# Optimization experiments

Measured on AMD Instinct MI355X. Metric: run time of the kernel, lower is better.

The kernel has to match this reference:

```python
import jax, jax.numpy as jnp
import numpy as np

D_IN = 4097   # 4096 obj feat + 1 depth
D_H1 = 512
D_H2 = 256
N_HEADS = 4
D_HEAD = D_H2 // N_HEADS
D_FF = 512


def setup_inputs() -> dict:
    key = jax.random.key(0)
    ks = jax.random.split(key, 20)
    B, T, N = 2, 100, 30
    s = lambda *sh: 1.0 / np.sqrt(sh[0])
    inp = {
        "object_features": jax.random.normal(ks[0], (B, T, N, 4096), jnp.float32),
        "object_depths": jax.random.uniform(ks[1], (B, T, N, 1), jnp.float32),
        # spatial encoder (2-layer fully-connected message passing)
        "W1a": jax.random.normal(ks[2], (D_IN, D_H1), jnp.float32) * s(D_IN),
        "W2a": jax.random.normal(ks[3], (D_IN, D_H1), jnp.float32) * s(D_IN),
        "b1a": jnp.zeros((D_H1,), jnp.float32),
        "W1b": jax.random.normal(ks[4], (D_H1, D_H2), jnp.float32) * s(D_H1),
        "W2b": jax.random.normal(ks[5], (D_H1, D_H2), jnp.float32) * s(D_H1),
        "b1b": jnp.zeros((D_H2,), jnp.float32),
        # temporal transformer encoder layer (post-LN)
        "Wq": jax.random.normal(ks[6], (D_H2, D_H2), jnp.float32) * s(D_H2),
        "Wk": jax.random.normal(ks[7], (D_H2, D_H2), jnp.float32) * s(D_H2),
        "Wv": jax.random.normal(ks[8], (D_H2, D_H2), jnp.float32) * s(D_H2),
        "Wo": jax.random.normal(ks[9], (D_H2, D_H2), jnp.float32) * s(D_H2),
        "ln1_g": jnp.ones((D_H2,), jnp.float32),
        "ln1_b": jnp.zeros((D_H2,), jnp.float32),
        "Wf1": jax.random.normal(ks[10], (D_H2, D_FF), jnp.float32) * s(D_H2),
        "bf1": jnp.zeros((D_FF,), jnp.float32),
        "Wf2": jax.random.normal(ks[11], (D_FF, D_H2), jnp.float32) * s(D_FF),
        "bf2": jnp.zeros((D_H2,), jnp.float32),
        "ln2_g": jnp.ones((D_H2,), jnp.float32),
        "ln2_b": jnp.zeros((D_H2,), jnp.float32),
        # classifier
        "Wc": jax.random.normal(ks[12], (D_H2, 1), jnp.float32) * s(D_H2),
        "bc": jnp.zeros((1,), jnp.float32),
    }
    return inp


def _layer_norm(x, g, b, eps=1e-5):
    mu = jnp.mean(x, axis=-1, keepdims=True)
    var = jnp.var(x, axis=-1, keepdims=True)
    return (x - mu) * jax.lax.rsqrt(var + eps) * g + b


def _forward(object_features, object_depths, W1a, W2a, b1a, W1b, W2b, b1b,
             Wq, Wk, Wv, Wo, ln1_g, ln1_b, Wf1, bf1, Wf2, bf2, ln2_g, ln2_b,
             Wc, bc):
    B, T, N, _ = object_features.shape
    x = jnp.concatenate([object_features, object_depths], axis=-1)  # (B,T,N,4097)
    # fully-connected graph (torch.combinations, both directions):
    # aggregated message for node i = mean over all j != i.
    def mp(h, Ws, Wn, b):
        neigh = (jnp.sum(h, axis=2, keepdims=True) - h) / (N - 1)
        return jax.nn.relu(h @ Ws + neigh @ Wn + b)
    h = mp(x, W1a, W2a, b1a)      # (B,T,N,512)
    h = mp(h, W1b, W2b, b1b)      # (B,T,N,256)
    g = jnp.mean(h, axis=2)       # global mean pool -> (B,T,256)
    # temporal transformer encoder (self-attention over T, post-LN)
    q = (g @ Wq).reshape(B, T, N_HEADS, D_HEAD)
    k = (g @ Wk).reshape(B, T, N_HEADS, D_HEAD)
    v = (g @ Wv).reshape(B, T, N_HEADS, D_HEAD)
    scores = jnp.einsum("bthd,bshd->bhts", q, k) / np.sqrt(D_HEAD)
    attn = jax.nn.softmax(scores, axis=-1)
    ctx = jnp.einsum("bhts,bshd->bthd", attn, v).reshape(B, T, D_H2) @ Wo
    y = _layer_norm(g + ctx, ln1_g, ln1_b)
    ff = jax.nn.relu(y @ Wf1 + bf1) @ Wf2 + bf2
    z = _layer_norm(y + ff, ln2_g, ln2_b)  # (B,T,256)
    # dropout is identity in eval mode -> probs2 == probs, uncertainty == 0
    logits = (z @ Wc + bc).squeeze(-1)     # (B,T)
    probs = jax.nn.sigmoid(logits)
    uncertainty = jnp.zeros_like(probs)
    return probs, uncertainty


def reference(object_features, object_depths, W1a, W2a, b1a, W1b, W2b, b1b,
              Wq, Wk, Wv, Wo, ln1_g, ln1_b, Wf1, bf1, Wf2, bf2, ln2_g, ln2_b,
              Wc, bc):
    return _forward(object_features, object_depths, W1a, W2a, b1a, W1b, W2b,
                    b1b, Wq, Wk, Wv, Wo, ln1_g, ln1_b, Wf1, bf1, Wf2, bf2,
                    ln2_g, ln2_b, Wc, bc)
```

## Files before the change

kernel.cpp:

```cpp
#include <hip/hip_runtime.h>
#include <hip/hip_bf16.h>
#include <stdint.h>

typedef unsigned short u16;
typedef __attribute__((ext_vector_type(8))) short short8;
typedef __attribute__((ext_vector_type(4))) float floatx4;

#define BT 200
#define NOBJ 30
#define KP2 4224
#define DIN 4097
#define DH1 512
#define DH2 256
#define DFF 512
#define MPAD 6016
#define CHZ 176
#define NBIGW (132*16)
#define NSMALL 512
#define NCONV (BT*12)
#define NZERO 128

__device__ __forceinline__ u16 f2bf(float f) {
    union { float f; uint32_t u; } c; c.f = f;
    uint32_t u = c.u;
    u += 0x7FFF + ((u >> 16) & 1);
    return (u16)(u >> 16);
}

__device__ __forceinline__ void load16_lds(const u16* g, u16* l) {
    __builtin_amdgcn_global_load_lds(
        (const __attribute__((address_space(1))) void*)g,
        (__attribute__((address_space(3))) void*)l, 16, 0, 0);
}

__device__ __forceinline__ size_t tile_off(int ytile, int row, int c8) {
    int z = c8 / CHZ, rem = c8 - z * CHZ;
    int i = rem >> 3, kw = rem & 7;
    int ks = kw ^ (row & 7);
    return ((((size_t)(ytile * 3 + z) * 22 + i) * 128 + row) * 64) + ks * 8;
}

__global__ void prep_all(const float* __restrict__ W1a, const float* __restrict__ W2a,
                         const float* __restrict__ W1b, const float* __restrict__ W2b,
                         const float* __restrict__ feat, const float* __restrict__ depth,
                         u16* __restrict__ Wc1T, u16* __restrict__ W2aTs,
                         u16* __restrict__ Wc2T, u16* __restrict__ W2bTs,
                         u16* __restrict__ XbT, u16* __restrict__ SbT,
                         float* __restrict__ zeroBase, size_t zeroQuads) {
    __shared__ float t1[32][33];
    __shared__ float t2[32][33];
    int bid = blockIdx.x, tid = threadIdx.x;
    if (bid < NBIGW) {
        int kb = (bid % 132) * 32, jb = (bid / 132) * 32;
        int tx = tid & 31, ty = tid >> 5;
        #pragma unroll
        for (int r = 0; r < 32; r += 8) {
            int k = kb + ty + r, j = jb + tx;
            float a = 0.f, b = 0.f;
            if (k < DIN) { a = W1a[k * DH1 + j]; b = W2a[k * DH1 + j]; }
            float bs = b * (1.f / 29.f);
            t1[ty + r][tx] = a - bs;
            t2[ty + r][tx] = bs;
        }
        __syncthreads();
        #pragma unroll
        for (int r = 0; r < 32; r += 8) {
            int j = jb + ty + r, k = kb + tx;
            int x = j >> 7, row = j & 127;
            size_t off = tile_off(x, row, k >> 3) + (k & 7);
            Wc1T[off]  = f2bf(t1[tx][ty + r]);
            W2aTs[off] = f2bf(t2[tx][ty + r]);
        }
    } else if (bid < NBIGW + NSMALL) {
        int idx = (bid - NBIGW) * 256 + tid;
        int j = idx >> 9, k = idx & 511;
        float a = W1b[k * DH2 + j];
        float b = W2b[k * DH2 + j] * (1.f / 29.f);
        Wc2T[j * DH1 + k]  = f2bf(a - b);
        W2bTs[j * DH1 + k] = f2bf(b);
    } else if (bid < NBIGW + NSMALL + NCONV) {
        int cid = bid - NBIGW - NSMALL;
        int slice = cid & 3, part = (cid >> 2) % 3, bt = cid / 12;
        int c8 = part * 256 + tid;
        if (c8 >= 528) return;
        const int nsA[4] = {0, 8, 16, 23};
        const int neA[4] = {8, 16, 23, 30};
        int k8 = c8 * 8;
        float s[8] = {};
        for (int n = nsA[slice]; n < neA[slice]; n++) {
            int r = bt * NOBJ + n;
            float v[8];
            if (k8 + 7 < 4096) {
                float4 a = *(const float4*)(feat + (size_t)r * 4096 + k8);
                float4 b = *(const float4*)(feat + (size_t)r * 4096 + k8 + 4);
                v[0]=a.x; v[1]=a.y; v[2]=a.z; v[3]=a.w;
                v[4]=b.x; v[5]=b.y; v[6]=b.z; v[7]=b.w;
            } else {
                #pragma unroll
                for (int e = 0; e < 8; e++) v[e] = 0.f;
                if (k8 == 4096) v[0] = depth[r];
            }
            short8 o;
            #pragma unroll
            for (int e = 0; e < 8; e++) { s[e] += v[e]; o[e] = (short)f2bf(v[e]); }
            *(short8*)(XbT + tile_off(r >> 7, r & 127, c8)) = o;
        }
        short8 so;
        #pragma unroll
        for (int e = 0; e < 8; e++) so[e] = (short)f2bf(s[e]);
        int grow = slice * 256 + bt;
        *(short8*)(SbT + tile_off(grow >> 7, grow & 127, c8)) = so;
    } else {
        int zid = bid - NBIGW - NSMALL - NCONV;
        float4* p = (float4*)zeroBase;
        float4 zz = {0.f, 0.f, 0.f, 0.f};
        for (size_t idx = (size_t)zid * 256 + tid; idx < zeroQuads; idx += (size_t)NZERO * 256)
            p[idx] = zz;
    }
}

__global__ __launch_bounds__(256) void gemmA(
    const u16* __restrict__ XbT, const u16* __restrict__ WaT,
    const u16* __restrict__ SbT, const u16* __restrict__ WsT,
    float* __restrict__ hacc, float* __restrict__ uOut) {
    __shared__ __align__(16) u16 Al[8192];
    __shared__ __align__(16) u16 Bl[8192];
    int bid = blockIdx.x;
    const u16 *Abase, *Bbase;
    float* outF;
    int m0, n0, seg0 = bid < 564;
    if (seg0) {
        int x = bid & 3, y = (bid >> 2) % 47, z = bid / 188;
        Abase = XbT + (size_t)((y * 3 + z) * 22) * 8192;
        Bbase = WaT + (size_t)((x * 3 + z) * 22) * 8192;
        outF = hacc; m0 = y * 128; n0 = x * 128;
    } else {
        int rem = bid - 564;
        int x = rem & 3, y = (rem >> 2) & 7, z = rem >> 5;
        Abase = SbT + (size_t)((y * 3 + z) * 22) * 8192;
        Bbase = WsT + (size_t)((x * 3 + z) * 22) * 8192;
        outF = uOut; m0 = y * 128; n0 = x * 128;
    }
    int tid = threadIdx.x, lane = tid & 63, w = tid >> 6;
    floatx4 acc[4][4] = {};
    int lrow = lane & 15, q = lane >> 4;
    int wm = (w & 1) * 64, wn = (w >> 1) * 64;
    int swz = lrow & 7;

    for (int i = 0; i < 22; i++) {
        const u16* as = Abase + (size_t)i * 8192;
        const u16* bs = Bbase + (size_t)i * 8192;
        #pragma unroll
        for (int it = 0; it < 4; it++) {
            load16_lds(as + (it * 256 + tid) * 8, Al + it * 2048 + w * 512);
            load16_lds(bs + (it * 256 + tid) * 8, Bl + it * 2048 + w * 512);
        }
        __syncthreads();
        #pragma unroll
        for (int h = 0; h < 2; h++) {
            int so = ((h * 4 + q) ^ swz) * 8;
            short8 af[4], bfv[4];
            #pragma unroll
            for (int ii = 0; ii < 4; ii++)
                af[ii] = *(short8*)(Al + (wm + ii * 16 + lrow) * 64 + so);
            #pragma unroll
            for (int j = 0; j < 4; j++)
                bfv[j] = *(short8*)(Bl + (wn + j * 16 + lrow) * 64 + so);
            #pragma unroll
            for (int ii = 0; ii < 4; ii++)
                #pragma unroll
                for (int j = 0; j < 4; j++)
                    acc[ii][j] = __builtin_amdgcn_mfma_f32_16x16x32_bf16(af[ii], bfv[j], acc[ii][j], 0, 0, 0);
        }
        __syncthreads();
    }

    #pragma unroll
    for (int ii = 0; ii < 4; ii++)
        #pragma unroll
        for (int j = 0; j < 4; j++)
            #pragma unroll
            for (int r = 0; r < 4; r++) {
                int row = m0 + wm + ii * 16 + q * 4 + r;
                int col = n0 + wn + j * 16 + lrow;
                if (seg0) {
                    if (row < 6000)
                        atomicAdd(&outF[(size_t)row * DH1 + col], acc[ii][j][r]);
                } else {
                    int urow = row & 255;
                    if (urow < BT)
                        atomicAdd(&outF[(size_t)urow * DH1 + col], acc[ii][j][r]);
                }
            }
}

__global__ __launch_bounds__(256) void gemmB(
    const u16* __restrict__ hb, const u16* __restrict__ Wc2T,
    const u16* __restrict__ Shb, const u16* __restrict__ W2bTs,
    float* __restrict__ hacc2, float* __restrict__ u2Out) {
    __shared__ __align__(16) u16 Al[64 * 64];
    __shared__ __align__(16) u16 Bl[128 * 64];
    int bid = blockIdx.x;
    const u16 *A, *B;
    float* outF;
    int m0, n0, kbeg, M;
    if (bid < 752) {
        int x = bid & 1, y = (bid >> 1) % 94, z = bid / 188;
        A = hb; B = Wc2T; outF = hacc2; M = 6000;
        m0 = y * 64; n0 = x * 128; kbeg = z * 128;
    } else {
        int rem = bid - 752;
        int x = rem & 1, y = (rem >> 1) & 3, z = rem >> 3;
        A = Shb; B = W2bTs; outF = u2Out; M = BT;
        m0 = y * 64; n0 = x * 128; kbeg = z * 128;
    }
    int kend = kbeg + 128;
    const int N = DH2, K = DH1;
    int tid = threadIdx.x;
    int lane = tid & 63, w = tid >> 6;
    int srow = tid >> 3, kslot = tid & 7;
    floatx4 acc[2][4] = {};
    int lrow = lane & 15, q = lane >> 4;
    int wm = (w & 1) * 32, wn = (w >> 1) * 64;
    int swz = lrow & 7;

    for (int kb = kbeg; kb < kend; kb += 64) {
        #pragma unroll
        for (int it = 0; it < 2; it++) {
            int row = it * 32 + srow;
            int kph = kslot ^ (row & 7);
            load16_lds(A + (size_t)(m0 + row) * K + kb + kph * 8,
                       Al + it * 2048 + w * 512);
        }
        #pragma unroll
        for (int it = 0; it < 4; it++) {
            int row = it * 32 + srow;
            int kph = kslot ^ (row & 7);
            load16_lds(B + (size_t)(n0 + row) * K + kb + kph * 8,
                       Bl + it * 2048 + w * 512);
        }
        __syncthreads();
        #pragma unroll
        for (int h = 0; h < 2; h++) {
            int so = ((h * 4 + q) ^ swz) * 8;
            short8 af[2], bfv[4];
            #pragma unroll
            for (int i = 0; i < 2; i++)
                af[i] = *(short8*)(Al + (wm + i * 16 + lrow) * 64 + so);
            #pragma unroll
            for (int j = 0; j < 4; j++)
                bfv[j] = *(short8*)(Bl + (wn + j * 16 + lrow) * 64 + so);
            #pragma unroll
            for (int i = 0; i < 2; i++)
                #pragma unroll
                for (int j = 0; j < 4; j++)
                    acc[i][j] = __builtin_amdgcn_mfma_f32_16x16x32_bf16(af[i], bfv[j], acc[i][j], 0, 0, 0);
        }
        __syncthreads();
    }

    #pragma unroll
    for (int i = 0; i < 2; i++)
        #pragma unroll
        for (int j = 0; j < 4; j++)
            #pragma unroll
            for (int r = 0; r < 4; r++) {
                int row = m0 + wm + i * 16 + q * 4 + r;
                int col = n0 + wn + j * 16 + lrow;
                if (row < M)
                    atomicAdd(&outF[(size_t)row * N + col], acc[i][j][r]);
            }
}

__global__ void reduce1(const float* __restrict__ hacc, const float* __restrict__ u,
                        const float* __restrict__ b1a,
                        u16* __restrict__ hb, u16* __restrict__ Shb) {
    __shared__ float sl[128];
    int bt = blockIdx.x, c0 = blockIdx.y * 128;
    int lc = threadIdx.x & 127, rp = threadIdx.x >> 7;
    int col = c0 + lc;
    float ub = u[bt * DH1 + col] + b1a[col];
    float s = 0.f;
    for (int n = rp; n < NOBJ; n += 2) {
        float v = hacc[(size_t)(bt * NOBJ + n) * DH1 + col] + ub;
        v = v > 0.f ? v : 0.f;
        hb[(size_t)(bt * NOBJ + n) * DH1 + col] = f2bf(v);
        s += v;
    }
    if (rp == 0) sl[lc] = s;
    __syncthreads();
    if (rp == 1) Shb[bt * DH1 + col] = f2bf(sl[lc] + s);
}

__global__ void reduce2_qkv(const float* __restrict__ hacc2, const float* __restrict__ u2,
                            const float* __restrict__ b1b,
                            const float* __restrict__ Wq, const float* __restrict__ Wk,
                            const float* __restrict__ Wv,
                            float* __restrict__ g, float* __restrict__ q,
                            float* __restrict__ k, float* __restrict__ v) {
    __shared__ float gl[DH2];
    int bt = blockIdx.x, j = threadIdx.x;
    float ub = u2[bt * DH2 + j] + b1b[j];
    float a = 0.f;
    for (int n = 0; n < NOBJ; n++) {
        float vv = hacc2[(size_t)(bt * NOBJ + n) * DH2 + j] + ub;
        a += vv > 0.f ? vv : 0.f;
    }
    a *= (1.f / 30.f);
    gl[j] = a;
    g[bt * DH2 + j] = a;
    __syncthreads();
    float aq = 0.f, ak = 0.f, av = 0.f;
    for (int kk = 0; kk < DH2; kk++) {
        float x = gl[kk];
        aq += x * Wq[kk * DH2 + j];
        ak += x * Wk[kk * DH2 + j];
        av += x * Wv[kk * DH2 + j];
    }
    q[bt * DH2 + j] = aq;
    k[bt * DH2 + j] = ak;
    v[bt * DH2 + j] = av;
}

__device__ __forceinline__ float block_sum256(float v, volatile float* red) {
    #pragma unroll
    for (int o = 32; o > 0; o >>= 1) v += __shfl_down(v, o);
    int w = threadIdx.x >> 6;
    __syncthreads();
    if ((threadIdx.x & 63) == 0) red[w] = v;
    __syncthreads();
    return red[0] + red[1] + red[2] + red[3];
}

__global__ void attn_head(const float* __restrict__ qg, const float* __restrict__ kg,
                          const float* __restrict__ vg, const float* __restrict__ g,
                          const float* __restrict__ Wo,
                          const float* __restrict__ ln1g, const float* __restrict__ ln1b,
                          const float* __restrict__ Wf1, const float* __restrict__ bf1,
                          const float* __restrict__ Wf2, const float* __restrict__ bf2,
                          const float* __restrict__ ln2g, const float* __restrict__ ln2b,
                          const float* __restrict__ Wc, const float* __restrict__ bc,
                          float* __restrict__ out) {
    __shared__ float ql[DH2];
    __shared__ float scl[4][128];
    __shared__ float ctxl[DH2];
    __shared__ float yl[DH2];
    __shared__ float ffl[DFF];
    __shared__ float red[4];
    int row = blockIdx.x, tid = threadIdx.x;
    int base = (row >= 100) ? 100 : 0;
    ql[tid] = qg[row * DH2 + tid];
    __syncthreads();

    for (int p = tid; p < 512; p += 256) {
        int h = p >> 7, s = p & 127;
        if (s < 100) {
            const float* kr = kg + (size_t)(base + s) * DH2 + h * 64;
            float a = 0.f;
            #pragma unroll 8
            for (int d = 0; d < 64; d++) a += ql[h * 64 + d] * kr[d];
            scl[h][s] = a * 0.125f;
        }
    }
    __syncthreads();

    {
        int w = tid >> 6, lane = tid & 63;
        int s2 = 64 + lane;
        float a  = scl[w][lane];
        float b2 = (s2 < 100) ? scl[w][s2] : -1e30f;
        float m = fmaxf(a, b2);
        #pragma unroll
        for (int o = 32; o > 0; o >>= 1) m = fmaxf(m, __shfl_down(m, o));
        m = __shfl(m, 0);
        float e1 = __expf(a - m);
        float e2 = (s2 < 100) ? __expf(b2 - m) : 0.f;
        float sm = e1 + e2;
        #pragma unroll
        for (int o = 32; o > 0; o >>= 1) sm += __shfl_down(sm, o);
        sm = __shfl(sm, 0);
        float r = 1.f / sm;
        scl[w][lane] = e1 * r;
        if (s2 < 100) scl[w][s2] = e2 * r;
    }
    __syncthreads();

    {
        int h = tid >> 6;
        float o = 0.f;
        for (int s = 0; s < 100; s++)
            o += scl[h][s] * vg[(size_t)(base + s) * DH2 + tid];
        ctxl[tid] = o;
    }
    __syncthreads();

    float o = 0.f;
    for (int kk = 0; kk < DH2; kk++) o += ctxl[kk] * Wo[kk * DH2 + tid];
    float t = g[row * DH2 + tid] + o;
    float mu  = block_sum256(t, red) * (1.f / DH2);
    float ex2 = block_sum256(t * t, red) * (1.f / DH2);
    float y = (t - mu) * rsqrtf(ex2 - mu * mu + 1e-5f) * ln1g[tid] + ln1b[tid];
    yl[tid] = y;
    __syncthreads();
    for (int jj = tid; jj < DFF; jj += 256) {
        float a = bf1[jj];
        for (int kk = 0; kk < DH2; kk++) a += yl[kk] * Wf1[kk * DFF + jj];
        ffl[jj] = a > 0.f ? a : 0.f;
    }
    __syncthreads();
    float o2 = bf2[tid];
    for (int kk = 0; kk < DFF; kk++) o2 += ffl[kk] * Wf2[kk * DH2 + tid];
    float z0 = y + o2;
    float mu2  = block_sum256(z0, red) * (1.f / DH2);
    float ex22 = block_sum256(z0 * z0, red) * (1.f / DH2);
    float z = (z0 - mu2) * rsqrtf(ex22 - mu2 * mu2 + 1e-5f) * ln2g[tid] + ln2b[tid];
    float logit = block_sum256(z * Wc[tid], red) + bc[0];
    if (tid == 0) {
        out[row]      = 1.f / (1.f + __expf(-logit));
        out[BT + row] = 0.f;
    }
}

extern "C" void kernel_launch(void* const* d_in, const int* in_sizes, int n_in,
                              void* d_out, int out_size, void* d_ws, size_t ws_size,
                              hipStream_t stream) {
    const float* feat  = (const float*)d_in[0];
    const float* depth = (const float*)d_in[1];
    const float* W1a = (const float*)d_in[2];
    const float* W2a = (const float*)d_in[3];
    const float* b1a = (const float*)d_in[4];
    const float* W1b = (const float*)d_in[5];
    const float* W2b = (const float*)d_in[6];
    const float* b1b = (const float*)d_in[7];
    const float* Wq  = (const float*)d_in[8];
    const float* Wk  = (const float*)d_in[9];
    const float* Wv  = (const float*)d_in[10];
    const float* Wo  = (const float*)d_in[11];
    const float* ln1g = (const float*)d_in[12];
    const float* ln1b = (const float*)d_in[13];
    const float* Wf1 = (const float*)d_in[14];
    const float* bf1 = (const float*)d_in[15];
    const float* Wf2 = (const float*)d_in[16];
    const float* bf2 = (const float*)d_in[17];
    const float* ln2g = (const float*)d_in[18];
    const float* ln2b = (const float*)d_in[19];
    const float* Wc  = (const float*)d_in[20];
    const float* bc  = (const float*)d_in[21];
    float* out = (float*)d_out;
    char* ws = (char*)d_ws;

    size_t off = 0;
    u16* XbT   = (u16*)(ws + off); off += (size_t)MPAD * KP2 * 2;
    u16* SbT   = (u16*)(ws + off); off += (size_t)1024 * KP2 * 2;
    u16* Wc1T  = (u16*)(ws + off); off += (size_t)DH1 * KP2 * 2;
    u16* W2aTs = (u16*)(ws + off); off += (size_t)DH1 * KP2 * 2;
    u16* Wc2T  = (u16*)(ws + off); off += (size_t)DH2 * DH1 * 2;
    u16* W2bTs = (u16*)(ws + off); off += (size_t)DH2 * DH1 * 2;
    u16* Shb   = (u16*)(ws + off); off += (size_t)256 * DH1 * 2;
    char* zBase = ws + off;
    float* hacc  = (float*)(ws + off); off += (size_t)6000 * DH1 * 4;
    float* hacc2 = (float*)(ws + off); off += (size_t)6000 * DH2 * 4;
    float* u     = (float*)(ws + off); off += (size_t)256 * DH1 * 4;
    float* u2    = (float*)(ws + off); off += (size_t)256 * DH2 * 4;
    size_t zeroQuads = (size_t)(ws + off - zBase) / 16;
    u16* hb = XbT;
    float* g = (float*)SbT;
    float* q = g + BT * DH2;
    float* k = q + BT * DH2;
    float* v = k + BT * DH2;

    prep_all<<<NBIGW + NSMALL + NCONV + NZERO, 256, 0, stream>>>(
        W1a, W2a, W1b, W2b, feat, depth,
        Wc1T, W2aTs, Wc2T, W2bTs, XbT, SbT, (float*)zBase, zeroQuads);
    gemmA<<<564 + 96, 256, 0, stream>>>(XbT, Wc1T, SbT, W2aTs, hacc, u);
    reduce1<<<dim3(BT, 4), 256, 0, stream>>>(hacc, u, b1a, hb, Shb);
    gemmB<<<752 + 32, 256, 0, stream>>>(hb, Wc2T, Shb, W2bTs, hacc2, u2);
    reduce2_qkv<<<BT, DH2, 0, stream>>>(hacc2, u2, b1b, Wq, Wk, Wv, g, q, k, v);
    attn_head<<<BT, DH2, 0, stream>>>(q, k, v, g, Wo, ln1g, ln1b, Wf1, bf1,
                                      Wf2, bf2, ln2g, ln2b, Wc, bc, out);
}
```

Before: 393.2 us.

## Double split-K in gemmA and coalesce prep writes through LDS staging

Splits the K dimension of the first GEMM into 6 chunks of 11 tiles instead of 3 chunks of 22, doubling the gemmA grid so more blocks run concurrently on the GPU. The tiled layout function changes to match. The weight transpose in prep now writes 16-byte vectors instead of scalar u16 stores. The feature conversion stages rows in LDS and writes whole contiguous tile rows. The cost is more atomic or partial-sum traffic into hacc and a shorter K loop per block, which leaves less to amortise each block's setup.

Result: slower. 418.5 us (+6.4%).

```diff
diff --git a/kernel.cpp b/kernel.cpp
--- a/kernel.cpp
+++ b/kernel.cpp
@@ -14,7 +14,6 @@
 #define DH2 256
 #define DFF 512
 #define MPAD 6016
-#define CHZ 176
 #define NBIGW (132*16)
 #define NSMALL 512
 #define NCONV (BT*12)
@@ -34,10 +33,10 @@
 }
 
 __device__ __forceinline__ size_t tile_off(int ytile, int row, int c8) {
-    int z = c8 / CHZ, rem = c8 - z * CHZ;
+    int z = c8 / 88, rem = c8 - z * 88;
     int i = rem >> 3, kw = rem & 7;
     int ks = kw ^ (row & 7);
-    return ((((size_t)(ytile * 3 + z) * 22 + i) * 128 + row) * 64) + ks * 8;
+    return ((((size_t)(ytile * 6 + z) * 11 + i) * 128 + row) * 64) + ks * 8;
 }
 
 __global__ void prep_all(const float* __restrict__ W1a, const float* __restrict__ W2a,
@@ -47,10 +46,11 @@
                          u16* __restrict__ Wc2T, u16* __restrict__ W2bTs,
                          u16* __restrict__ XbT, u16* __restrict__ SbT,
                          float* __restrict__ zeroBase, size_t zeroQuads) {
-    __shared__ float t1[32][33];
-    __shared__ float t2[32][33];
+    __shared__ __align__(16) char smem[32768];
     int bid = blockIdx.x, tid = threadIdx.x;
     if (bid < NBIGW) {
+        float (*t1)[33] = (float(*)[33])smem;
+        float (*t2)[33] = (float(*)[33])(smem + 4352);
         int kb = (bid % 132) * 32, jb = (bid / 132) * 32;
         int tx = tid & 31, ty = tid >> 5;
         #pragma unroll
@@ -63,13 +63,17 @@
             t2[ty + r][tx] = bs;
         }
         __syncthreads();
-        #pragma unroll
-        for (int r = 0; r < 32; r += 8) {
-            int j = jb + ty + r, k = kb + tx;
-            int x = j >> 7, row = j & 127;
-            size_t off = tile_off(x, row, k >> 3) + (k & 7);
-            Wc1T[off]  = f2bf(t1[tx][ty + r]);
-            W2aTs[off] = f2bf(t2[tx][ty + r]);
+        {
+            int arr = tid >> 7, tt = tid & 127;
+            int jrel = tt >> 2, ch = tt & 3;
+            int j = jb + jrel;
+            float (*src)[33] = arr ? t2 : t1;
+            short8 o;
+            #pragma unroll
+            for (int e = 0; e < 8; e++) o[e] = (short)f2bf(src[ch * 8 + e][jrel]);
+            int c8 = (kb >> 3) + ch;
+            size_t off = tile_off(j >> 7, j & 127, c8);
+            *(short8*)((arr ? W2aTs : Wc1T) + off) = o;
         }
     } else if (bid < NBIGW + NSMALL) {
         int idx = (bid - NBIGW) * 256 + tid;
@@ -79,37 +83,57 @@
         Wc2T[j * DH1 + k]  = f2bf(a - b);
         W2bTs[j * DH1 + k] = f2bf(b);
     } else if (bid < NBIGW + NSMALL + NCONV) {
+        u16* st = (u16*)smem;
         int cid = bid - NBIGW - NSMALL;
         int slice = cid & 3, part = (cid >> 2) % 3, bt = cid / 12;
-        int c8 = part * 256 + tid;
-        if (c8 >= 528) return;
         const int nsA[4] = {0, 8, 16, 23};
         const int neA[4] = {8, 16, 23, 30};
-        int k8 = c8 * 8;
-        float s[8] = {};
-        for (int n = nsA[slice]; n < neA[slice]; n++) {
-            int r = bt * NOBJ + n;
-            float v[8];
-            if (k8 + 7 < 4096) {
-                float4 a = *(const float4*)(feat + (size_t)r * 4096 + k8);
-                float4 b = *(const float4*)(feat + (size_t)r * 4096 + k8 + 4);
-                v[0]=a.x; v[1]=a.y; v[2]=a.z; v[3]=a.w;
-                v[4]=b.x; v[5]=b.y; v[6]=b.z; v[7]=b.w;
-            } else {
+        int n0 = nsA[slice], ne = neA[slice], nrows = ne - n0;
+        int nci = (part < 2) ? 32 : 2;
+        int c8 = part * 256 + tid;
+        int valid = tid < nci * 8;
+        if (valid) {
+            int k8 = c8 * 8;
+            float s[8] = {};
+            int ci = tid >> 3, kw = tid & 7;
+            for (int n = n0; n < ne; n++) {
+                int r = bt * NOBJ + n;
+                float v[8];
+                if (k8 + 7 < 4096) {
+                    float4 a = *(const float4*)(feat + (size_t)r * 4096 + k8);
+                    float4 b = *(const float4*)(feat + (size_t)r * 4096 + k8 + 4);
+                    v[0]=a.x; v[1]=a.y; v[2]=a.z; v[3]=a.w;
+                    v[4]=b.x; v[5]=b.y; v[6]=b.z; v[7]=b.w;
+                } else {
+                    #pragma unroll
+                    for (int e = 0; e < 8; e++) v[e] = 0.f;
+                    if (k8 == 4096) v[0] = depth[r];
+                }
+                short8 o;
                 #pragma unroll
-                for (int e = 0; e < 8; e++) v[e] = 0.f;
-                if (k8 == 4096) v[0] = depth[r];
+                for (int e = 0; e < 8; e++) { s[e] += v[e]; o[e] = (short)f2bf(v[e]); }
+                *(short8*)&st[(((size_t)(n - n0) * 32 + ci) * 8 + kw) * 8] = o;
             }
-            short8 o;
-            #pragma unroll
-            for (int e = 0; e < 8; e++) { s[e] += v[e]; o[e] = (short)f2bf(v[e]); }
-            *(short8*)(XbT + tile_off(r >> 7, r & 127, c8)) = o;
-        }
-        short8 so;
-        #pragma unroll
-        for (int e = 0; e < 8; e++) so[e] = (short)f2bf(s[e]);
-        int grow = slice * 256 + bt;
-        *(short8*)(SbT + tile_off(grow >> 7, grow & 127, c8)) = so;
+            short8 so;
+            #pragma unroll
+            for (int e = 0; e < 8; e++) so[e] = (short)f2bf(s[e]);
+            int grow = slice * 256 + bt;
+            *(short8*)(SbT + tile_off(grow >> 7, grow & 127, c8)) = so;
+        }
+        __syncthreads();
+        int nchunks = nci * 64;
+        for (int cidx = tid; cidx < nchunks; cidx += 256) {
+            int ci = cidx >> 6, rem = cidx & 63;
+            int rr = rem >> 3, s = rem & 7;
+            if (rr >= nrows) continue;
+            int r = bt * NOBJ + n0 + rr;
+            int row = r & 127, tile = r >> 7;
+            int c8g = part * 256 + ci * 8;
+            int z = c8g / 88, i = (c8g % 88) >> 3;
+            int kw = s ^ (row & 7);
+            short8 val = *(short8*)&st[(((size_t)rr * 32 + ci) * 8 + kw) * 8];
+            *(short8*)(XbT + ((((size_t)(tile * 6 + z) * 11 + i) * 128 + row) * 64 + s * 8)) = val;
+        }
     } else {
         int zid = bid - NBIGW - NSMALL - NCONV;
         float4* p = (float4*)zeroBase;
@@ -128,17 +152,17 @@
     int bid = blockIdx.x;
     const u16 *Abase, *Bbase;
     float* outF;
-    int m0, n0, seg0 = bid < 564;
+    int m0, n0, seg0 = bid < 1128;
     if (seg0) {
         int x = bid & 3, y = (bid >> 2) % 47, z = bid / 188;
-        Abase = XbT + (size_t)((y * 3 + z) * 22) * 8192;
-        Bbase = WaT + (size_t)((x * 3 + z) * 22) * 8192;
+        Abase = XbT + (size_t)((y * 6 + z) * 11) * 8192;
+        Bbase = WaT + (size_t)((x * 6 + z) * 11) * 8192;
         outF = hacc; m0 = y * 128; n0 = x * 128;
     } else {
-        int rem = bid - 564;
+        int rem = bid - 1128;
         int x = rem & 3, y = (rem >> 2) & 7, z = rem >> 5;
-        Abase = SbT + (size_t)((y * 3 + z) * 22) * 8192;
-        Bbase = WsT + (size_t)((x * 3 + z) * 22) * 8192;
+        Abase = SbT + (size_t)((y * 6 + z) * 11) * 8192;
+        Bbase = WsT + (size_t)((x * 6 + z) * 11) * 8192;
         outF = uOut; m0 = y * 128; n0 = x * 128;
     }
     int tid = threadIdx.x, lane = tid & 63, w = tid >> 6;
@@ -147,7 +171,7 @@
     int wm = (w & 1) * 64, wn = (w >> 1) * 64;
     int swz = lrow & 7;
 
-    for (int i = 0; i < 22; i++) {
+    for (int i = 0; i < 11; i++) {
         const u16* as = Abase + (size_t)i * 8192;
         const u16* bs = Bbase + (size_t)i * 8192;
         #pragma unroll
@@ -472,7 +496,7 @@
     prep_all<<<NBIGW + NSMALL + NCONV + NZERO, 256, 0, stream>>>(
         W1a, W2a, W1b, W2b, feat, depth,
         Wc1T, W2aTs, Wc2T, W2bTs, XbT, SbT, (float*)zBase, zeroQuads);
-    gemmA<<<564 + 96, 256, 0, stream>>>(XbT, Wc1T, SbT, W2aTs, hacc, u);
+    gemmA<<<1128 + 192, 256, 0, stream>>>(XbT, Wc1T, SbT, W2aTs, hacc, u);
     reduce1<<<dim3(BT, 4), 256, 0, stream>>>(hacc, u, b1a, hb, Shb);
     gemmB<<<752 + 32, 256, 0, stream>>>(hb, Wc2T, Shb, W2bTs, hacc2, u2);
     reduce2_qkv<<<BT, DH2, 0, stream>>>(hacc2, u2, b1b, Wq, Wk, Wv, g, q, k, v);
```
